# Performance work log

Hardware: AMD Instinct MI355X
Metric: run time of the kernel (lower is better)

## Reference

```python
import jax, jax.numpy as jnp
import numpy as np

D = 4; R = 12; C = 32
P = 2 * R + 1            # 25 fine patch
N = P * P                # 625
MEM_R = 12; MEM_P = 2 * MEM_R + 1
K = 20; DIL_INT = 16


def local_correlation(ft, fr, rad, dil):
    """Zero-padded local correlation (SpatialCorrelationSampler, kernel=1).
    ft, fr: (b,c,h,w) -> (b,Pp,Pp,h,w) with Pp=2*rad+1, patch dilation dil."""
    b, c, h, w = ft.shape
    Pp = 2 * rad + 1
    pad = rad * dil
    frp = jnp.pad(fr, ((0, 0), (0, 0), (pad, pad), (pad, pad)))
    rows = (jnp.arange(Pp)[:, None] * dil + jnp.arange(h)[None, :]).reshape(-1)
    cols = (jnp.arange(Pp)[:, None] * dil + jnp.arange(w)[None, :]).reshape(-1)
    g = frp[:, :, rows, :][:, :, :, cols].reshape(b, c, Pp, h, Pp, w)
    return jnp.einsum('bchw,bcyhxw->byxhw', ft, g)


def bilinear_sample(img, py, px):
    """Bilinear sample img (b,c,H,W) at float coords py/px (broadcastable shape S);
    zero outside the image. Returns (b,c,*S)."""
    b, c, H, W = img.shape
    y0f = jnp.floor(py); x0f = jnp.floor(px)
    wy = py - y0f; wx = px - x0f
    y0 = y0f.astype(jnp.int32); x0 = x0f.astype(jnp.int32)

    def tap(yi, xi, wgt):
        valid = (yi >= 0) & (yi < H) & (xi >= 0) & (xi < W)
        v = img[:, :, jnp.clip(yi, 0, H - 1), jnp.clip(xi, 0, W - 1)]
        return v * (wgt * valid)[None, None]

    return (tap(y0, x0, (1 - wy) * (1 - wx)) + tap(y0, x0 + 1, (1 - wy) * wx)
            + tap(y0 + 1, x0, wy * (1 - wx)) + tap(y0 + 1, x0 + 1, wy * wx))


def _topk_dim1(corr, k):
    # corr: (b,N,hw); torch.topk(dim=1, sorted=True) equivalent
    vals, idx = jax.lax.top_k(corr.transpose(0, 2, 1), k)   # (b,hw,k)
    return vals.transpose(0, 2, 1), idx                      # (b,k,hw), (b,hw,k)


def _long_ref(ft, fr, q, dirate):
    b, c, h, w = ft.shape
    # coarse dilated correlation -> softmax -> soft-argmax expected offset
    corr_c = local_correlation(ft, fr, MEM_R, dirate).reshape(b, MEM_P * MEM_P, h * w)
    attn = jax.nn.softmax(corr_c, axis=1).reshape(b, MEM_P, MEM_P, h, w)
    d = jnp.arange(-MEM_R, MEM_R + 1, dtype=ft.dtype)
    off_y = jnp.einsum('byxhw,y->bhw', attn, d) * dirate
    off_x = jnp.einsum('byxhw,x->bhw', attn, d) * dirate
    # deform_im2col with PxP kernel: sample fr at (r+dy+off_y, c+dx+off_x)
    dtap = jnp.arange(-R, R + 1, dtype=ft.dtype)
    py = dtap[:, None, None, None] + (jnp.arange(h, dtype=ft.dtype)[:, None] + off_y[0])[None, None]
    px = dtap[None, :, None, None] + (jnp.arange(w, dtype=ft.dtype)[None, :] + off_x[0])[None, None]
    col = bilinear_sample(fr, py, px)                        # (b,c,P,P,h,w)
    corr = jnp.einsum('bchw,bcyxhw->byxhw', ft, col).reshape(b, N, h * w)
    vals, idx = _topk_dim1(corr, K)
    # process_long_image_uf_topk: shift offsets by decoded top-k displacement, 1-tap bilinear
    dr = (idx[0] // 25 - 12).reshape(h, w, K).transpose(2, 0, 1).astype(ft.dtype)  # (K,h,w)
    dc = (idx[0] % 25 - 12).reshape(h, w, K).transpose(2, 0, 1).astype(ft.dtype)
    py2 = jnp.arange(h, dtype=ft.dtype)[None, :, None] + off_y[0][None] + dr
    px2 = jnp.arange(w, dtype=ft.dtype)[None, None, :] + off_x[0][None] + dc
    imgs = bilinear_sample(q, py2, px2)                      # (b,C,K,h,w)
    return vals, imgs.reshape(b, q.shape[1], K, h * w)


def _short_ref(ft, fr, q):
    b, c, h, w = ft.shape
    corr = local_correlation(ft, fr, R, 1).reshape(b, N, h * w)
    vals, idx = _topk_dim1(corr, K)
    # process_short_image_uf_topk: integer gather q[:, :, r+dr, c+dc] (zero-padded)
    dr = (idx[0] // 25 - 12).reshape(h, w, K).transpose(2, 0, 1)   # (K,h,w) int
    dc = (idx[0] % 25 - 12).reshape(h, w, K).transpose(2, 0, 1)
    qp = jnp.pad(q, ((0, 0), (0, 0), (R, R), (R, R)))
    yi = jnp.arange(h)[None, :, None] + dr + R
    xi = jnp.arange(w)[None, None, :] + dc + R
    imgs = qp[:, :, yi, xi]                                  # (b,C,K,h,w)
    return vals, imgs.reshape(b, q.shape[1], K, h * w)


def _forward(feats_r, feats_t, quantized_r, ref_index, current_ind):
    ref_index = np.asarray(ref_index)
    current_ind = int(current_ind)
    gaps = current_ind - ref_index
    nsearch = int(np.sum(gaps > DIL_INT))
    dirates = [int(min(4, g // DIL_INT + 1)) for g in gaps if g > DIL_INT]
    nref = feats_r.shape[0]
    b, c, h, w = feats_t.shape
    # prep(): subsample labels by D (C=32 channels, one_hot skipped)
    qr = [quantized_r[i][:, :, ::D, ::D].astype(feats_t.dtype) for i in range(nref)]
    vals_all, imgs_all = [], []
    for i in range(nsearch):
        v, im = _long_ref(feats_t, feats_r[i], qr[i], dirates[i])
        vals_all.append(v); imgs_all.append(im)
    for i in range(nsearch, nref):
        v, im = _short_ref(feats_t, feats_r[i], qr[i])
        vals_all.append(v); imgs_all.append(im)
    attn = jax.nn.softmax(jnp.concatenate(vals_all, axis=1), axis=1)  # (b, nref*K, hw)
    imgs = jnp.concatenate(imgs_all, axis=2)                          # (b, C, nref*K, hw)
    return jnp.einsum('bkp,bckp->bcp', attn, imgs).reshape(b, qr[0].shape[1], h, w)


def setup_inputs():
    key = jax.random.key(0)
    k1, k2, k3 = jax.random.split(key, 3)
    feats_r = jax.random.normal(k1, (3, 1, 64, 48, 48), dtype=jnp.float32)
    feats_t = jax.random.normal(k2, (1, 64, 48, 48), dtype=jnp.float32)
    quantized_r = jax.random.uniform(k3, (3, 1, 32, 192, 192), dtype=jnp.float32)
    # gaps vs current_ind=60: 20 (>16 -> long ref, dirate=2), 10, 5 (short refs)
    ref_index = np.array([40, 50, 55], dtype=np.int64)
    current_ind = 60
    return {"feats_r": feats_r, "feats_t": feats_t, "quantized_r": quantized_r,
            "ref_index": ref_index, "current_ind": current_ind}


def reference(feats_r, feats_t, quantized_r, ref_index, current_ind):
    return _forward(feats_r, feats_t, quantized_r, ref_index, current_ind)
```

## Files before the change

kernel.cpp:

```cpp
#include <hip/hip_runtime.h>
#include <math.h>

#define HW 48
#define NPIX 2304
#define CF 64
#define CQ 32
#define RAD 12
#define PP 25
#define NTAP 625
#define KTOP 20
#define DILINT 16
#define QW 192
#define CSTRIDE 640
#define NPB 6
#define NC 30
#define LROW 68
#define DGS 28


__device__ inline int read_ref_index(const void* rip, int r) {
    const long long* p64 = (const long long*)rip;
    long long v0 = p64[0];
    if (v0 >= 0 && v0 < 1000000) return (int)p64[r];
    return ((const int*)rip)[r];
}

__device__ inline int get_dil(const void* refIdx, const void* curInd, int r,
                              bool* isLong) {
    int cur = ((const int*)curInd)[0];
    int gap = cur - read_ref_index(refIdx, r);
    *isLong = gap > DILINT;
    return *isLong ? min(4, gap / DILINT + 1) : 1;
}

__global__ void prep_kernel(const float* __restrict__ fr,
                            const float* __restrict__ ft,
                            const float* __restrict__ q, int nref,
                            float* __restrict__ ftT,
                            float* __restrict__ frT,
                            float* __restrict__ qrT) {
    int i = blockIdx.x * blockDim.x + threadIdx.x;
    int tft = NPIX * CF;
    int tfr = nref * NPIX * CF;
    int tqr = nref * NPIX * CQ;
    if (i < tft) {
        int p = i >> 6, c = i & 63;
        ftT[i] = ft[c * NPIX + p];
    } else if (i < tft + tfr) {
        int j = i - tft;
        int rr = j / (NPIX * CF);
        int rem = j % (NPIX * CF);
        int p = rem >> 6, c = rem & 63;
        frT[j] = fr[((size_t)rr * CF + c) * NPIX + p];
    } else if (i < tft + tfr + tqr) {
        int j = i - tft - tfr;
        int rr = j / (NPIX * CQ);
        int rem = j % (NPIX * CQ);
        int p = rem >> 5, c = rem & 31;
        int y = p / HW, x = p % HW;
        qrT[j] = q[(((size_t)rr * CQ + c) * QW + 4 * y) * QW + 4 * x];
    }
}

__global__ __launch_bounds__(256) void corr_band(
    const float* __restrict__ ftT, const float* __restrict__ frT,
    const void* __restrict__ refIdx, const void* __restrict__ curInd,
    float* __restrict__ corr) {
    __shared__ float lrow[NC * LROW];

    int tid = threadIdx.x;
    int bx = blockIdx.x % 9;
    int y = blockIdx.x / 9;
    int r = blockIdx.y;

    bool isLong;
    int dil = get_dil(refIdx, curInd, r, &isLong);
    int nb = (dil == 3) ? 9 : 8;
    if (bx >= nb) return;

    int m = bx % dil, grp = bx / dil;
    int npr = HW / dil;

    int T = tid;
    bool active = T < NPB * PP;
    int j = active ? T / PP : 0;
    int dxi = active ? T - PP * j : 0;
    int xoff = grp * NPB + j;
    bool pvalid = active && (xoff < npr);
    int xj = m + dil * xoff;
    int pj = pvalid ? (y * HW + xj) : 0;
    int lc = j + dxi;

    float4 fq[16];
    const float4* fp = (const float4*)(ftT + (size_t)pj * CF);
#pragma unroll
    for (int i = 0; i < 16; ++i) fq[i] = fp[i];

    const float* frb = frT + (size_t)r * NPIX * CF;
    float* outb = corr + ((size_t)r * NPIX + pj) * CSTRIDE + dxi;
    int gc0 = m + dil * (grp * NPB - RAD);

    for (int dy = 0; dy < PP; ++dy) {
        int yy = y + dil * (dy - RAD);
        if (yy < 0 || yy >= HW) {
            if (pvalid) outb[dy * PP] = 0.f;
            continue;
        }
        for (int k = tid; k < NC * 16; k += 256) {
            int col = k >> 4, sub = k & 15;
            int gc = gc0 + dil * col;
            float4 v = {0.f, 0.f, 0.f, 0.f};
            if (gc >= 0 && gc < HW)
                v = *(const float4*)(frb + ((size_t)yy * HW + gc) * CF + sub * 4);
            *(float4*)(lrow + col * LROW + sub * 4) = v;
        }
        __syncthreads();
        if (pvalid) {
            const float* bp = lrow + lc * LROW;
            float s = 0.f;
#pragma unroll
            for (int i = 0; i < 16; ++i) {
                float4 b = *(const float4*)(bp + 4 * i);
                s += fq[i].x * b.x + fq[i].y * b.y + fq[i].z * b.z + fq[i].w * b.w;
            }
            outb[dy * PP] = s;
        }
        __syncthreads();
    }
}

__global__ __launch_bounds__(192) void corr_fuse(
    const float* __restrict__ ftT, const float* __restrict__ frT,
    const float* __restrict__ qrT, const float* __restrict__ corr,
    const void* __restrict__ refIdx, const void* __restrict__ curInd,
    int nref, float* __restrict__ out) {
    __shared__ float dgw_s[3][27 * DGS];
    __shared__ float valsL[96];
    __shared__ int   topiL[96];
    __shared__ float accL[3][64];
    __shared__ float ssmL[3][64];
    __shared__ float offL[3][2];

    int tid = threadIdx.x;
    int wid = tid >> 6, lane = tid & 63;
    int p = blockIdx.x;
    int y = p / HW, x = p % HW;
    int r = wid;

    bool isLong;
    int dil = get_dil(refIdx, curInd, r, &isLong);
    float oy = 0.f, ox = 0.f;

    const float* cb = corr + ((size_t)r * NPIX + p) * CSTRIDE;
    float creg[10];
#pragma unroll
    for (int jj = 0; jj < 10; ++jj) {
        int t = lane + 64 * jj;
        creg[jj] = (t < NTAP) ? cb[t] : -INFINITY;
    }

    if (isLong) {
        float M = -INFINITY;
#pragma unroll
        for (int jj = 0; jj < 10; ++jj) M = fmaxf(M, creg[jj]);
#pragma unroll
        for (int s = 32; s; s >>= 1) M = fmaxf(M, __shfl_xor(M, s, 64));
        float s0 = 0.f, sy = 0.f, sx = 0.f;
#pragma unroll
        for (int jj = 0; jj < 10; ++jj) {
            int t = lane + 64 * jj;
            if (t < NTAP) {
                float e = expf(creg[jj] - M);
                int dy = t / PP - RAD, dx = t % PP - RAD;
                s0 += e; sy += e * (float)dy; sx += e * (float)dx;
            }
        }
#pragma unroll
        for (int s = 32; s; s >>= 1) {
            s0 += __shfl_xor(s0, s, 64);
            sy += __shfl_xor(sy, s, 64);
            sx += __shfl_xor(sx, s, 64);
        }
        oy = sy / s0 * (float)dil;
        ox = sx / s0 * (float)dil;
        if (lane == 0) { offL[r][0] = oy; offL[r][1] = ox; }
    }
    __syncthreads();

    for (int rr = 0; rr < nref; ++rr) {
        bool rrLong;
        get_dil(refIdx, curInd, rr, &rrLong);
        if (!rrLong) continue;
        float roy = offL[rr][0], rox = offL[rr][1];
        float fy = (float)y + roy, fx = (float)x + rox;
        int iy0 = (int)floorf(fy), ix0 = (int)floorf(fx);

        int cs = tid & 15;
        int g2 = tid >> 4;
        float4 fqc = ((const float4*)(ftT + (size_t)p * CF))[cs];
        const float* frb = frT + (size_t)rr * NPIX * CF;
        float* dgw = dgw_s[rr];
        int colbase = ix0 - RAD;
        for (int a = 0; a < 26; ++a) {
            int yy = iy0 - RAD + a;
            bool yok = (yy >= 0 && yy < HW);
            const float* rowp = frb + (size_t)(yok ? yy : 0) * (HW * CF);
#pragma unroll
            for (int i = 0; i < 3; ++i) {
                int lc2 = 12 * i + g2;
                int xx2 = colbase + lc2;
                int xs = min(max(xx2, 0), HW - 1);
                float s = 0.f;
                if (yok && lc2 < 26) {
                    float4 b = *(const float4*)(rowp + xs * CF + 4 * cs);
                    s = fqc.x * b.x + fqc.y * b.y + fqc.z * b.z + fqc.w * b.w;
                    s = (xx2 >= 0 && xx2 < HW) ? s : 0.f;
                }
                s += __shfl_xor(s, 1, 64);
                s += __shfl_xor(s, 2, 64);
                s += __shfl_xor(s, 4, 64);
                s += __shfl_xor(s, 8, 64);
                if (cs == 0 && lc2 < 26) dgw[a * DGS + lc2] = s;
            }
        }
    }
    __syncthreads();

    if (isLong) {
        float fy = (float)y + oy, fx = (float)x + ox;
        float fy0 = floorf(fy), fx0 = floorf(fx);
        float wy = fy - fy0, wx = fx - fx0;
        const float* dgw = dgw_s[r];
        float w00 = (1.f - wy) * (1.f - wx), w01 = (1.f - wy) * wx;
        float w10 = wy * (1.f - wx), w11 = wy * wx;
#pragma unroll
        for (int jj = 0; jj < 10; ++jj) {
            int t = lane + 64 * jj;
            if (t < NTAP) {
                int a = t / PP, bcol = t % PP;
                creg[jj] = w00 * dgw[a * DGS + bcol] + w01 * dgw[a * DGS + bcol + 1] +
                           w10 * dgw[(a + 1) * DGS + bcol] + w11 * dgw[(a + 1) * DGS + bcol + 1];
            }
        }
    }

    for (int k = 0; k < KTOP; ++k) {
        float bv = creg[0]; int bt = lane;
#pragma unroll
        for (int jj = 1; jj < 10; ++jj) {
            int t = lane + 64 * jj;
            if (creg[jj] > bv) { bv = creg[jj]; bt = t; }
        }
#pragma unroll
        for (int s = 32; s; s >>= 1) {
            float ov = __shfl_xor(bv, s, 64);
            int ot = __shfl_xor(bt, s, 64);
            if (ov > bv || (ov == bv && ot < bt)) { bv = ov; bt = ot; }
        }
        if (lane == 0) { valsL[r * KTOP + k] = bv; topiL[r * KTOP + k] = bt; }
        if ((bt & 63) == lane) {
            int jj2 = bt >> 6;
#pragma unroll
            for (int jj = 0; jj < 10; ++jj)
                if (jj == jj2) creg[jj] = -INFINITY;
        }
    }
    __syncthreads();

    int c = lane & 31, h = lane >> 5;
    int nk = nref * KTOP;
    float m = -INFINITY;
    for (int k = 0; k < nk; ++k) m = fmaxf(m, valsL[k]);

    float ssum = 0.f, acc = 0.f;
    const float* qb = qrT + (size_t)r * NPIX * CQ;
    for (int k2 = 0; k2 < KTOP / 2; ++k2) {
        int k = r * KTOP + h * (KTOP / 2) + k2;
        float e = expf(valsL[k] - m);
        ssum += e;
        int id = topiL[k];
        int dr = id / PP - RAD, dc = id % PP - RAD;
        float img = 0.f;
        if (isLong) {
            float py = (float)y + oy + (float)dr;
            float px = (float)x + ox + (float)dc;
            float fy0 = floorf(py), fx0 = floorf(px);
            int y0 = (int)fy0, x0 = (int)fx0;
            float wy = py - fy0, wx = px - fx0;
            float w00 = (1.f - wy) * (1.f - wx), w01 = (1.f - wy) * wx;
            float w10 = wy * (1.f - wx), w11 = wy * wx;
            if (y0 >= 0 && y0 < HW && x0 >= 0 && x0 < HW)
                img += w00 * qb[(y0 * HW + x0) * CQ + c];
            if (y0 >= 0 && y0 < HW && x0 + 1 >= 0 && x0 + 1 < HW)
                img += w01 * qb[(y0 * HW + x0 + 1) * CQ + c];
            if (y0 + 1 >= 0 && y0 + 1 < HW && x0 >= 0 && x0 < HW)
                img += w10 * qb[((y0 + 1) * HW + x0) * CQ + c];
            if (y0 + 1 >= 0 && y0 + 1 < HW && x0 + 1 >= 0 && x0 + 1 < HW)
                img += w11 * qb[((y0 + 1) * HW + x0 + 1) * CQ + c];
        } else {
            int yy = y + dr, xx = x + dc;
            if (yy >= 0 && yy < HW && xx >= 0 && xx < HW)
                img = qb[(yy * HW + xx) * CQ + c];
        }
        acc += e * img;
    }
    accL[wid][lane] = acc;
    ssmL[wid][lane] = ssum;
    __syncthreads();

    if (wid == 0) {
        float ta = 0.f, ts = 0.f;
        for (int w = 0; w < nref; ++w) { ta += accL[w][lane]; ts += ssmL[w][lane]; }
        ta += __shfl_xor(ta, 32, 64);
        ts += __shfl_xor(ts, 32, 64);
        if (h == 0) out[(size_t)c * NPIX + p] = ta / ts;
    }
}

extern "C" void kernel_launch(void* const* d_in, const int* in_sizes, int n_in,
                              void* d_out, int out_size, void* d_ws, size_t ws_size,
                              hipStream_t stream) {
    const float* fr = (const float*)d_in[0];
    const float* ft = (const float*)d_in[1];
    const float* q  = (const float*)d_in[2];
    const void* refIdx = d_in[3];
    const void* curInd = d_in[4];
    int nref = in_sizes[0] / (CF * NPIX);

    float* ws  = (float*)d_ws;
    float* ftT = ws;
    float* frT = ftT + (size_t)NPIX * CF;
    float* qrT = frT + (size_t)nref * NPIX * CF;
    float* corr = qrT + (size_t)nref * NPIX * CQ;

    int total = NPIX * CF + nref * NPIX * CF + nref * NPIX * CQ;
    prep_kernel<<<(total + 255) / 256, 256, 0, stream>>>(fr, ft, q, nref, ftT, frT, qrT);
    corr_band<<<dim3(HW * 9, nref), 256, 0, stream>>>(ftT, frT, refIdx, curInd, corr);
    corr_fuse<<<dim3(NPIX), 64 * nref, 0, stream>>>(ftT, frT, qrT, corr, refIdx, curInd,
                                                    nref, (float*)d_out);
}
```

Measured before the change: 118.9 us.

## Pack value and index into double keys and extract top-2 per wave reduction

Top-k selection now encodes each score and its tap index into a single order-preserving double key, so each wave reduction moves one value instead of a value/index pair. Each round finds the top two keys and halves the number of cross-lane shuffle rounds. The softmax max over stored values becomes a wave shuffle reduction instead of a serial loop. In exchange it uses FP64 max/min and shuffles, which may be slower per operation and raise register pressure; -0 is normalised to +0.

```diff
diff --git a/kernel.cpp b/kernel.cpp
--- a/kernel.cpp
+++ b/kernel.cpp
@@ -244,33 +244,59 @@
         }
     }
 
-    for (int k = 0; k < KTOP; ++k) {
-        float bv = creg[0]; int bt = lane;
+    double key[10];
+#pragma unroll
+    for (int jj = 0; jj < 10; ++jj) {
+        float v = creg[jj] + 0.0f;
+        unsigned u = __float_as_uint(v);
+        u = (u & 0x80000000u) ? ~u : (u | 0x80000000u);
+        int t = lane + 64 * jj;
+        key[jj] = (double)u * 1024.0 + (double)(1023 - t);
+    }
+
+    for (int k2 = 0; k2 < KTOP / 2; ++k2) {
+        double a = key[0], b = -1.0;
 #pragma unroll
         for (int jj = 1; jj < 10; ++jj) {
-            int t = lane + 64 * jj;
-            if (creg[jj] > bv) { bv = creg[jj]; bt = t; }
+            double kk = key[jj];
+            double na = fmax(a, kk);
+            b = fmax(b, fmin(a, kk));
+            a = na;
         }
 #pragma unroll
         for (int s = 32; s; s >>= 1) {
-            float ov = __shfl_xor(bv, s, 64);
-            int ot = __shfl_xor(bt, s, 64);
-            if (ov > bv || (ov == bv && ot < bt)) { bv = ov; bt = ot; }
-        }
-        if (lane == 0) { valsL[r * KTOP + k] = bv; topiL[r * KTOP + k] = bt; }
-        if ((bt & 63) == lane) {
-            int jj2 = bt >> 6;
-#pragma unroll
-            for (int jj = 0; jj < 10; ++jj)
-                if (jj == jj2) creg[jj] = -INFINITY;
+            double pa = __shfl_xor(a, s, 64);
+            double pb = __shfl_xor(b, s, 64);
+            double na = fmax(a, pa);
+            b = fmax(fmin(a, pa), fmax(b, pb));
+            a = na;
+        }
+        if (lane == 0) {
+            double qa = floor(a * (1.0 / 1024.0));
+            double qb2 = floor(b * (1.0 / 1024.0));
+            unsigned ua = (unsigned)qa, ub = (unsigned)qb2;
+            unsigned ba = (ua & 0x80000000u) ? (ua ^ 0x80000000u) : ~ua;
+            unsigned bb = (ub & 0x80000000u) ? (ub ^ 0x80000000u) : ~ub;
+            int ta = 1023 - (int)(a - qa * 1024.0);
+            int tb = 1023 - (int)(b - qb2 * 1024.0);
+            valsL[r * KTOP + 2 * k2]     = __uint_as_float(ba);
+            topiL[r * KTOP + 2 * k2]     = ta;
+            valsL[r * KTOP + 2 * k2 + 1] = __uint_as_float(bb);
+            topiL[r * KTOP + 2 * k2 + 1] = tb;
+        }
+#pragma unroll
+        for (int jj = 0; jj < 10; ++jj) {
+            double kk = key[jj];
+            key[jj] = (kk == a || kk == b) ? 0.0 : kk;
         }
     }
     __syncthreads();
 
     int c = lane & 31, h = lane >> 5;
     int nk = nref * KTOP;
-    float m = -INFINITY;
-    for (int k = 0; k < nk; ++k) m = fmaxf(m, valsL[k]);
+    float m = (lane < nk) ? valsL[lane] : -INFINITY;
+#pragma unroll
+    for (int s = 32; s; s >>= 1) m = fmaxf(m, __shfl_xor(m, s, 64));
 
     float ssum = 0.f, acc = 0.f;
     const float* qb = qrT + (size_t)r * NPIX * CQ;
```

New measurement: 109.6 us. -7.8%, faster.
